# Kernel tuning notes

Hardware: AMD Instinct MI355X
Metric: run time of the kernel (lower is better)

## Reference

```python
import jax, jax.numpy as jnp
from jax import lax
import numpy as np


def _conv(x, w, b, groups=1):
    # x: NCHW, w: OIHW, stride 1, SAME padding
    y = lax.conv_general_dilated(x, w, (1, 1), 'SAME',
                                 dimension_numbers=('NCHW', 'OIHW', 'NCHW'),
                                 feature_group_count=groups)
    return y + b[None, :, None, None]


def setup_inputs() -> dict:
    key = jax.random.key(0)
    ks = jax.random.split(key, 9)
    B, C, H, W, N, K = 8, 64, 256, 256, 10, 64
    f = lambda k, s, sc=0.05: jax.random.normal(k, s, dtype=jnp.float32) * sc
    return dict(
        x=jax.random.normal(ks[0], (B, C, H, W), dtype=jnp.float32),
        ln_g=jnp.ones((C,), jnp.float32), ln_b=jnp.zeros((C,), jnp.float32),
        conv3_w=f(ks[1], (C, C, 3, 3)), conv3_b=jnp.zeros((C,), jnp.float32),
        dw_w=f(ks[2], (C, 1, 3, 3)), dw_b=jnp.zeros((C,), jnp.float32),
        c1_w=f(ks[3], (C, C, 1, 1)), c1_b=jnp.zeros((C,), jnp.float32),
        c2_w=f(ks[4], (N, C, 1, 1)), c2_b=jnp.zeros((N,), jnp.float32),
        base=f(ks[5], (N, K, K), 1.0),
        up_w=f(ks[6], (K, C, 3, 3)), up_b=jnp.zeros((K,), jnp.float32),
        down_w=f(ks[7], (C, K, 3, 3)), down_b=jnp.zeros((C,), jnp.float32),
    )


def reference(x, ln_g, ln_b, conv3_w, conv3_b, dw_w, dw_b, c1_w, c1_b,
              c2_w, c2_b, base, up_w, up_b, down_w, down_b):
    eps = 1e-5
    # LayerNorm over channel dim (permute(0,2,3,1) -> LN(last) -> permute back)
    mu = jnp.mean(x, axis=1, keepdims=True)
    var = jnp.var(x, axis=1, keepdims=True)
    xn = (x - mu) / jnp.sqrt(var + eps) * ln_g[None, :, None, None] + ln_b[None, :, None, None]
    x1 = jax.nn.gelu(_conv(xn, conv3_w, conv3_b), approximate=False)
    # predict module: dwconv -> GAP -> 1x1 -> relu -> 1x1 -> softmax over N
    C = x.shape[1]
    p = _conv(x1, dw_w, dw_b, groups=C)
    p = jnp.mean(p, axis=(2, 3), keepdims=True)           # [B,C,1,1]
    p = jax.nn.relu(_conv(p, c1_w, c1_b))
    p = _conv(p, c2_w, c2_b)[:, :, 0, 0]                  # [B,N]
    w = jax.nn.softmax(p, axis=1)                         # [B,N]
    # blend N basis KxK matrices per sample
    Wm = jnp.einsum('bn,nkl->bkl', w, base)               # [B,K,K]
    xm = _conv(x1, up_w, up_b)                            # [B,K,H,W]
    B, K, H, Wd = xm.shape
    xm = jnp.einsum('bkl,bkm->blm', Wm, xm.reshape(B, K, H * Wd)).reshape(B, K, H, Wd)
    xm = _conv(xm, down_w, down_b)                        # [B,C,H,W]
    return x + xm
```

## Files before the change

kernel.cpp:

```cpp
#include <hip/hip_runtime.h>
#include <math.h>

constexpr int B = 8, C = 64, H = 256, W = 256, HWc = H * W, N = 10;

typedef short bf8 __attribute__((ext_vector_type(8)));
typedef float f4  __attribute__((ext_vector_type(4)));
typedef unsigned short ushort;

__device__ __forceinline__ ushort f2bf(float f) {
  unsigned u = __builtin_bit_cast(unsigned, f);
  unsigned r = (u + 0x7fffu + ((u >> 16) & 1u)) >> 16;
  return (ushort)r;
}
__device__ __forceinline__ float bf2f(ushort h) {
  unsigned u = ((unsigned)h) << 16;
  return __builtin_bit_cast(float, u);
}

__global__ __launch_bounds__(256) void ln_k(
    const float* __restrict__ x, const float* __restrict__ g,
    const float* __restrict__ bt, ushort* __restrict__ xn) {
  int pix = blockIdx.x * 256 + threadIdx.x;
  int b = blockIdx.y;
  const float* xp = x + (size_t)b * C * HWc + pix;
  float v[64];
  float s = 0.f, s2 = 0.f;
#pragma unroll
  for (int c = 0; c < 64; c++) {
    v[c] = xp[(size_t)c * HWc];
    s += v[c]; s2 += v[c] * v[c];
  }
  float mu = s * (1.f / 64);
  float var = s2 * (1.f / 64) - mu * mu;
  float rstd = rsqrtf(var + 1e-5f);
  ushort* op = xn + ((size_t)b * HWc + pix) * 64;
#pragma unroll
  for (int ch = 0; ch < 8; ch++) {
    union { ushort us[8]; int4 v4; } pk;
#pragma unroll
    for (int j = 0; j < 8; j++) {
      int c = ch * 8 + j;
      pk.us[j] = f2bf((v[c] - mu) * rstd * g[c] + bt[c]);
    }
    *reinterpret_cast<int4*>(op + ch * 8) = pk.v4;
  }
}

__global__ void prep_w(const float* __restrict__ w3, const float* __restrict__ wu,
                       const float* __restrict__ wd, ushort* __restrict__ frags) {
  int idx = blockIdx.x * 256 + threadIdx.x;
  if (idx >= 3 * 4608) return;
  int conv = idx / 4608, r = idx % 4608;
  int s = r >> 8, cf = (r >> 6) & 3, lane = r & 63;
  const float* w = (conv == 0) ? w3 : (conv == 1) ? wu : wd;
  int co = (cf << 4) + (lane & 15);
  int tap = s >> 1;
  ushort* o = frags + conv * 36864 + ((size_t)r) * 8;
#pragma unroll
  for (int j = 0; j < 8; j++) {
    int ci = ((s & 1) << 5) + ((lane >> 4) << 3) + j;
    o[j] = f2bf(w[(co * 64 + ci) * 9 + tap]);
  }
}

struct Stg { int4 v[6]; };

__device__ __forceinline__ void stage_load(
    Stg& s, const ushort* __restrict__ in, int b, int h0, int w0,
    int ch2, int tid) {
#pragma unroll
  for (int it = 0; it < 6; it++) {
    int idx = it * 256 + tid;
    int4 v = make_int4(0, 0, 0, 0);
    if (idx < 1296) {
      int pix = idx >> 2, ch = idx & 3;
      int r = pix / 18, c = pix % 18;
      int gh = h0 + r - 1, gw = w0 + c - 1;
      if (gh >= 0 && gh < H && gw >= 0 && gw < W)
        v = *reinterpret_cast<const int4*>(
            in + (((size_t)b * H + gh) * W + gw) * 64 + ch2 * 32 + ch * 8);
    }
    s.v[it] = v;
  }
}

__device__ __forceinline__ void stage_write(const Stg& s, char* lds, int tid) {
#pragma unroll
  for (int it = 0; it < 6; it++) {
    int idx = it * 256 + tid;
    if (idx < 1296) {
      int pix = idx >> 2, ch = idx & 3;
      int c = pix % 18;
      int off = ((pix << 6) + (ch << 4)) ^ (((c >> 1) & 3) << 4);
      *reinterpret_cast<int4*>(lds + off) = s.v[it];
    }
  }
}

__device__ __forceinline__ void compute_half(
    const char* lds, const bf8* __restrict__ wf, int ch2,
    int wave, int lm, int lk, f4 (&acc)[16]) {
#pragma unroll
  for (int dx = 0; dx < 3; dx++) {
    bf8 wb3[3];
#pragma unroll
    for (int dy = 0; dy < 3; dy++) {
      int s = ((dy * 3 + dx) << 1) | ch2;
      wb3[dy] = wf[(s * 4 + wave) * 64 + (lk << 4) + lm];
    }
    int lc = lm + dx;
    int swz = ((lc >> 1) & 3) << 4;
#pragma unroll
    for (int hf = 0; hf < 2; hf++) {
      bf8 a[10];
#pragma unroll
      for (int r = 0; r < 10; r++) {
        int row = hf * 8 + r;
        int off = (((row * 18 + lc) << 6) + (lk << 4)) ^ swz;
        a[r] = *reinterpret_cast<const bf8*>(lds + off);
      }
#pragma unroll
      for (int dy = 0; dy < 3; dy++)
#pragma unroll
        for (int f = 0; f < 8; f++)
          acc[hf * 8 + f] =
              __builtin_amdgcn_mfma_f32_16x16x32_bf16(a[f + dy], wb3[dy], acc[hf * 8 + f], 0, 0, 0);
    }
  }
}

__device__ __forceinline__ void red_at(
    float* ldsf, const float (&a)[8], float* __restrict__ stats9,
    int k, int b, int tid) {
  __syncthreads();
#pragma unroll
  for (int j = 0; j < 8; j++) ldsf[j * 256 + tid] = a[j];
  __syncthreads();
  if (tid < 64) {
    float s = 0.f;
#pragma unroll
    for (int kk = 0; kk < 32; kk++) s += ldsf[(tid & 7) * 256 + kk * 8 + (tid >> 3)];
    atomicAdd(&stats9[(b * 64 + tid) * 9 + k], s);
  }
}

template <int ACT, int OM, int DOST>
__global__ __launch_bounds__(256, 2) void conv_mfma(
    const ushort* __restrict__ in, const ushort* __restrict__ wfrag,
    const float* __restrict__ bias, const float* __restrict__ resid,
    ushort* __restrict__ outb, float* __restrict__ outf,
    float* __restrict__ stats9) {
  __shared__ char lds[2 * 20736];
  char* ldsA = lds;
  char* ldsB = lds + 20736;
  int tid = threadIdx.x;
  int b = blockIdx.z;
  int h0 = blockIdx.y * 16, w0 = blockIdx.x * 16;
  int wave = tid >> 6, lane = tid & 63;
  int lm = lane & 15, lk = lane >> 4;
  const bf8* wf = reinterpret_cast<const bf8*>(wfrag);

  f4 acc[16];
  {
    float bv = bias[(wave << 4) + lm];
    f4 ini = {bv, bv, bv, bv};
#pragma unroll
    for (int f = 0; f < 16; f++) acc[f] = ini;
  }

  {
    Stg s0;
    stage_load(s0, in, b, h0, w0, 0, tid);
    stage_write(s0, ldsA, tid);
    __syncthreads();
  }
  {
    Stg s1;
    stage_load(s1, in, b, h0, w0, 1, tid);
    compute_half(ldsA, wf, 0, wave, lm, lk, acc);
    stage_write(s1, ldsB, tid);
    __syncthreads();
  }
  compute_half(ldsB, wf, 1, wave, lm, lk, acc);

  float* ldsf = reinterpret_cast<float*>(ldsA);
  if (OM == 0) {
    float s8[8];
    if (DOST) {
#pragma unroll
      for (int j = 0; j < 8; j++) s8[j] = 0.f;
    }
    for (int q = 0; q < 4; q++) {
      __syncthreads();
#pragma unroll
      for (int fr = 0; fr < 4; fr++) {
        int f = q * 4 + fr;
        int co = (wave << 4) + lm;
#pragma unroll
        for (int r = 0; r < 4; r++) {
          int p = (lk << 2) + r;
          ldsf[fr * 1024 + p * 64 + (co ^ ((p & 12) << 2))] = acc[f][r];
        }
      }
      __syncthreads();
#pragma unroll
      for (int i = 0; i < 2; i++) {
        int q2 = i * 256 + tid;
        int co8 = q2 & 7, p = (q2 >> 3) & 15, fr = q2 >> 7;
        int cb = (co8 * 8) ^ ((p & 12) << 2);
        f4 v0 = *reinterpret_cast<f4*>(&ldsf[fr * 1024 + p * 64 + cb]);
        f4 v1 = *reinterpret_cast<f4*>(&ldsf[fr * 1024 + p * 64 + cb + 4]);
        float vv[8] = {v0[0], v0[1], v0[2], v0[3], v1[0], v1[1], v1[2], v1[3]};
        union { ushort us[8]; int4 i4; } pk;
#pragma unroll
        for (int j = 0; j < 8; j++) {
          float v = vv[j];
          if (ACT) v = 0.5f * v * (1.f + erff(v * 0.70710678118654752f));
          if (DOST) s8[j] += v;
          pk.us[j] = f2bf(v);
        }
        *reinterpret_cast<int4*>(
            outb + (((size_t)b * H + h0 + q * 4 + fr) * W + w0 + p) * 64 + co8 * 8) = pk.i4;
      }
    }
    if (DOST) red_at(ldsf, s8, stats9, 0, b, tid);
  } else {
    for (int q = 0; q < 4; q++) {
      __syncthreads();
      if (wave == q) {
#pragma unroll
        for (int f = 0; f < 16; f++) {
          int pxl = (f << 4) + (lk << 2);
          int pxs = pxl ^ ((lm & 7) << 2);
          *reinterpret_cast<f4*>(&ldsf[lm * 256 + pxs]) = acc[f];
        }
      }
      float4 rv[4];
#pragma unroll
      for (int i = 0; i < 4; i++) {
        int q2 = i * 256 + tid;
        int chunk = q2 & 63, co16 = q2 >> 6;
        int pq = chunk * 4;
        int co = q * 16 + co16;
        size_t o = ((size_t)(b * 64 + co)) * HWc +
                   (size_t)(h0 + (pq >> 4)) * W + w0 + (pq & 15);
        rv[i] = *reinterpret_cast<const float4*>(resid + o);
      }
      __syncthreads();
#pragma unroll
      for (int i = 0; i < 4; i++) {
        int q2 = i * 256 + tid;
        int chunk = q2 & 63, co16 = q2 >> 6;
        int pq = chunk * 4;
        int pxs = pq ^ ((co16 & 7) << 2);
        f4 v = *reinterpret_cast<f4*>(&ldsf[co16 * 256 + pxs]);
        int co = q * 16 + co16;
        size_t o = ((size_t)(b * 64 + co)) * HWc +
                   (size_t)(h0 + (pq >> 4)) * W + w0 + (pq & 15);
        float4 ov;
        ov.x = v[0] + rv[i].x; ov.y = v[1] + rv[i].y;
        ov.z = v[2] + rv[i].z; ov.w = v[3] + rv[i].w;
        *reinterpret_cast<float4*>(outf + o) = ov;
      }
    }
  }
}

__global__ __launch_bounds__(256) void edge_k(const ushort* __restrict__ x1,
                                              float* __restrict__ stats9) {
  int b = blockIdx.x;
  int t = threadIdx.x;
  __shared__ float red[256];
  const size_t bb = (size_t)b * HWc * 64;
#pragma unroll
  for (int st = 0; st < 4; st++) {
    float s = 0.f;
    for (int i = 0; i < 64; i++) {
      int idx = i * 256 + t;
      int pix = idx >> 6, c = idx & 63;
      size_t off;
      if (st == 0)      off = ((size_t)pix) * 64 + c;
      else if (st == 1) off = ((size_t)(H - 1) * W + pix) * 64 + c;
      else if (st == 2) off = ((size_t)pix * W) * 64 + c;
      else              off = ((size_t)pix * W + (W - 1)) * 64 + c;
      s += bf2f(x1[bb + off]);
    }
    red[t] = s;
    __syncthreads();
    if (t < 64) {
      float v = red[t] + red[t + 64] + red[t + 128] + red[t + 192];
      stats9[(b * 64 + t) * 9 + 1 + st] = v;
    }
    __syncthreads();
  }
  if (t < 64) {
    stats9[(b * 64 + t) * 9 + 5] = bf2f(x1[bb + t]);
    stats9[(b * 64 + t) * 9 + 6] = bf2f(x1[bb + ((size_t)(W - 1)) * 64 + t]);
    stats9[(b * 64 + t) * 9 + 7] = bf2f(x1[bb + ((size_t)(H - 1) * W) * 64 + t]);
    stats9[(b * 64 + t) * 9 + 8] = bf2f(x1[bb + ((size_t)(H - 1) * W + W - 1) * 64 + t]);
  }
}

__global__ __launch_bounds__(256, 2) void upmix_mfma(
    const ushort* __restrict__ in, const ushort* __restrict__ wfrag,
    const float* __restrict__ bias, const ushort* __restrict__ wmf,
    ushort* __restrict__ out) {
  __shared__ char ldsS[20736];
  __shared__ char ldsX[32768];
  int tid = threadIdx.x;
  int b = blockIdx.z;
  int h0 = blockIdx.y * 16, w0 = blockIdx.x * 16;
  int wave = tid >> 6, lane = tid & 63;
  int lm = lane & 15, lk = lane >> 4;
  const bf8* wf = reinterpret_cast<const bf8*>(wfrag);

  const bf8* wmb = reinterpret_cast<const bf8*>(wmf + (size_t)b * 4096);
  bf8 wm[2];
#pragma unroll
  for (int s = 0; s < 2; s++) wm[s] = wmb[(s * 4 + wave) * 64 + lane];

  f4 acc[16];
  {
    float bv = bias[(wave << 4) + lm];
    f4 ini = {bv, bv, bv, bv};
#pragma unroll
    for (int f = 0; f < 16; f++) acc[f] = ini;
  }

  {
    Stg s0;
    stage_load(s0, in, b, h0, w0, 0, tid);
    stage_write(s0, ldsS, tid);
    __syncthreads();
  }
  {
    Stg s1;
    stage_load(s1, in, b, h0, w0, 1, tid);
    compute_half(ldsS, wf, 0, wave, lm, lk, acc);
    stage_write(s1, ldsX, tid);
    __syncthreads();
  }
  compute_half(ldsX, wf, 1, wave, lm, lk, acc);
  __syncthreads();

#pragma unroll
  for (int f = 0; f < 16; f++) {
#pragma unroll
    for (int r = 0; r < 4; r++) {
      int pc = (lk << 2) + r;
      int pix = (f << 4) + pc;
      int off = ((pix << 7) + ((wave << 4) + lm) * 2) ^ ((pc & 7) << 4);
      *reinterpret_cast<ushort*>(ldsX + off) = f2bf(acc[f][r]);
    }
  }
  __syncthreads();

  f4 acc2[16];
#pragma unroll
  for (int f = 0; f < 16; f++) acc2[f] = (f4){0.f, 0.f, 0.f, 0.f};
#pragma unroll
  for (int s = 0; s < 2; s++) {
    int kbyte = ((s << 5) + (lk << 3)) << 1;
#pragma unroll
    for (int f = 0; f < 16; f++) {
      int off = ((((f << 4) + lm) << 7) + kbyte) ^ ((lm & 7) << 4);
      bf8 a = *reinterpret_cast<const bf8*>(ldsX + off);
      acc2[f] = __builtin_amdgcn_mfma_f32_16x16x32_bf16(a, wm[s], acc2[f], 0, 0, 0);
    }
  }

  float* ldsf = reinterpret_cast<float*>(ldsS);
  for (int q = 0; q < 4; q++) {
    __syncthreads();
#pragma unroll
    for (int fr = 0; fr < 4; fr++) {
      int f = q * 4 + fr;
      int co = (wave << 4) + lm;
#pragma unroll
      for (int r = 0; r < 4; r++) {
        int p = (lk << 2) + r;
        ldsf[fr * 1024 + p * 64 + (co ^ ((p & 12) << 2))] = acc2[f][r];
      }
    }
    __syncthreads();
#pragma unroll
    for (int i = 0; i < 2; i++) {
      int q2 = i * 256 + tid;
      int co8 = q2 & 7, p = (q2 >> 3) & 15, fr = q2 >> 7;
      int cb = (co8 * 8) ^ ((p & 12) << 2);
      f4 v0 = *reinterpret_cast<f4*>(&ldsf[fr * 1024 + p * 64 + cb]);
      f4 v1 = *reinterpret_cast<f4*>(&ldsf[fr * 1024 + p * 64 + cb + 4]);
      float vv[8] = {v0[0], v0[1], v0[2], v0[3], v1[0], v1[1], v1[2], v1[3]};
      union { ushort us[8]; int4 i4; } pk;
#pragma unroll
      for (int j = 0; j < 8; j++) pk.us[j] = f2bf(vv[j]);
      *reinterpret_cast<int4*>(
          out + (((size_t)b * H + h0 + q * 4 + fr) * W + w0 + p) * 64 + co8 * 8) = pk.i4;
    }
  }
}

__global__ void mlp_k(const float* __restrict__ stats9, const float* __restrict__ dww,
                      const float* __restrict__ dwb,
                      const float* __restrict__ c1w, const float* __restrict__ c1b,
                      const float* __restrict__ c2w, const float* __restrict__ c2b,
                      const float* __restrict__ basep, ushort* __restrict__ wmf) {
  int b = blockIdx.x;
  int t = threadIdx.x;
  __shared__ float pm[64], p1[64], p2[16];
  {
    const float* st = stats9 + (b * 64 + t) * 9;
    float S = st[0], R0 = st[1], Rh = st[2], C0 = st[3], Cw = st[4];
    float X00 = st[5], X0w = st[6], Xh0 = st[7], Xhw = st[8];
    float acc = 0.f;
#pragma unroll
    for (int ky = 0; ky < 3; ky++)
#pragma unroll
      for (int kx = 0; kx < 3; kx++) {
        float T = S;
        if (ky == 2) T -= R0;
        if (ky == 0) T -= Rh;
        if (kx == 2) T -= C0;
        if (kx == 0) T -= Cw;
        if (ky == 2 && kx == 2) T += X00;
        if (ky == 2 && kx == 0) T += X0w;
        if (ky == 0 && kx == 2) T += Xh0;
        if (ky == 0 && kx == 0) T += Xhw;
        acc += dww[t * 9 + ky * 3 + kx] * T;
      }
    pm[t] = acc * (1.f / HWc) + dwb[t];
  }
  __syncthreads();
  float a = c1b[t];
  for (int ci = 0; ci < 64; ci++) a += pm[ci] * c1w[t * 64 + ci];
  p1[t] = fmaxf(a, 0.f);
  __syncthreads();
  if (t < N) {
    float a2 = c2b[t];
    for (int ci = 0; ci < 64; ci++) a2 += p1[ci] * c2w[t * 64 + ci];
    p2[t] = a2;
  }
  __syncthreads();
  float m = -1e30f;
  for (int n = 0; n < N; n++) m = fmaxf(m, p2[n]);
  float e[N], s = 0.f;
  for (int n = 0; n < N; n++) { e[n] = expf(p2[n] - m); s += e[n]; }
  float inv = 1.f / s;
  for (int idx = t; idx < 4096; idx += 64) {
    int j = idx & 7, lane = (idx >> 3) & 63, cf = (idx >> 9) & 3, s2 = idx >> 11;
    int k = (s2 << 5) + ((lane >> 4) << 3) + j;
    int l = (cf << 4) + (lane & 15);
    float acc = 0.f;
    for (int n = 0; n < N; n++) acc += e[n] * inv * basep[n * 4096 + k * 64 + l];
    wmf[(size_t)b * 4096 + idx] = f2bf(acc);
  }
}

__global__ void zero_k(float* p, int n) {
  int i = blockIdx.x * 256 + threadIdx.x;
  if (i < n) p[i] = 0.f;
}

extern "C" void kernel_launch(void* const* d_in, const int* in_sizes, int n_in,
                              void* d_out, int out_size, void* d_ws, size_t ws_size,
                              hipStream_t stream) {
  const float* x       = (const float*)d_in[0];
  const float* ln_g    = (const float*)d_in[1];
  const float* ln_b    = (const float*)d_in[2];
  const float* conv3_w = (const float*)d_in[3];
  const float* conv3_b = (const float*)d_in[4];
  const float* dw_w    = (const float*)d_in[5];
  const float* dw_b    = (const float*)d_in[6];
  const float* c1_w    = (const float*)d_in[7];
  const float* c1_b    = (const float*)d_in[8];
  const float* c2_w    = (const float*)d_in[9];
  const float* c2_b    = (const float*)d_in[10];
  const float* basep   = (const float*)d_in[11];
  const float* up_w    = (const float*)d_in[12];
  const float* up_b    = (const float*)d_in[13];
  const float* down_w  = (const float*)d_in[14];
  const float* down_b  = (const float*)d_in[15];
  float* out = (float*)d_out;

  char* wsb = (char*)d_ws;
  size_t big = (size_t)B * HWc * 64 * sizeof(ushort);
  ushort* bufA   = (ushort*)wsb;
  ushort* bufB   = (ushort*)(wsb + big);
  ushort* wfrags = (ushort*)(wsb + 2 * big);
  ushort* wmfrag = (ushort*)(wsb + 2 * big + 3 * 36864 * 2);
  float*  stats  = (float*)(wsb + 2 * big + 3 * 36864 * 2 + 8 * 4096 * 2);

  prep_w<<<54, 256, 0, stream>>>(conv3_w, up_w, down_w, wfrags);
  zero_k<<<18, 256, 0, stream>>>(stats, B * 64 * 9);
  ln_k<<<dim3(HWc / 256, B), 256, 0, stream>>>(x, ln_g, ln_b, bufA);
  conv_mfma<1, 0, 1><<<dim3(16, 16, B), 256, 0, stream>>>(
      bufA, wfrags + 0 * 36864, conv3_b, nullptr, bufB, nullptr, stats);
  edge_k<<<B, 256, 0, stream>>>(bufB, stats);
  mlp_k<<<B, 64, 0, stream>>>(stats, dw_w, dw_b, c1_w, c1_b, c2_w, c2_b, basep, wmfrag);
  upmix_mfma<<<dim3(16, 16, B), 256, 0, stream>>>(
      bufB, wfrags + 1 * 36864, up_b, wmfrag, bufA);
  conv_mfma<0, 1, 0><<<dim3(16, 16, B), 256, 0, stream>>>(
      bufA, wfrags + 2 * 36864, down_b, x, nullptr, out, stats);
}
```

Before: 331.5 us.

## Fuse edge stats into MLP kernel, write residual output directly, halve epilogue passes

Folds the edge/corner statistics kernel into the MLP kernel, which now runs 256 threads and keeps the intermediates in shared memory, so one launch and the global stats round-trip go away. The final conv epilogue no longer transposes through LDS: each lane reads the residual and writes float4 output straight from its accumulators. The bf16 epilogues of conv3 and upmix stage 8 rows per pass instead of 4, which halves the barrier rounds but uses more LDS. The direct residual path gives less coalesced 16-byte accesses per row in exchange for dropping the LDS shuffle and its syncs.

```diff
diff --git a/kernel.cpp b/kernel.cpp
--- a/kernel.cpp
+++ b/kernel.cpp
@@ -130,8 +130,8 @@
 }
 
 __device__ __forceinline__ void red_at(
-    float* ldsf, const float (&a)[8], float* __restrict__ stats9,
-    int k, int b, int tid) {
+    float* ldsf, const float (&a)[8], float* __restrict__ Ssum,
+    int b, int tid) {
   __syncthreads();
 #pragma unroll
   for (int j = 0; j < 8; j++) ldsf[j * 256 + tid] = a[j];
@@ -140,7 +140,7 @@
     float s = 0.f;
 #pragma unroll
     for (int kk = 0; kk < 32; kk++) s += ldsf[(tid & 7) * 256 + kk * 8 + (tid >> 3)];
-    atomicAdd(&stats9[(b * 64 + tid) * 9 + k], s);
+    atomicAdd(&Ssum[b * 64 + tid], s);
   }
 }
 
@@ -149,7 +149,7 @@
     const ushort* __restrict__ in, const ushort* __restrict__ wfrag,
     const float* __restrict__ bias, const float* __restrict__ resid,
     ushort* __restrict__ outb, float* __restrict__ outf,
-    float* __restrict__ stats9) {
+    float* __restrict__ Ssum) {
   __shared__ char lds[2 * 20736];
   char* ldsA = lds;
   char* ldsB = lds + 20736;
@@ -183,18 +183,18 @@
   }
   compute_half(ldsB, wf, 1, wave, lm, lk, acc);
 
-  float* ldsf = reinterpret_cast<float*>(ldsA);
   if (OM == 0) {
+    float* ldsf = reinterpret_cast<float*>(lds);
     float s8[8];
     if (DOST) {
 #pragma unroll
       for (int j = 0; j < 8; j++) s8[j] = 0.f;
     }
-    for (int q = 0; q < 4; q++) {
+    for (int h2 = 0; h2 < 2; h2++) {
       __syncthreads();
 #pragma unroll
-      for (int fr = 0; fr < 4; fr++) {
-        int f = q * 4 + fr;
+      for (int fr = 0; fr < 8; fr++) {
+        int f = h2 * 8 + fr;
         int co = (wave << 4) + lm;
 #pragma unroll
         for (int r = 0; r < 4; r++) {
@@ -204,7 +204,7 @@
       }
       __syncthreads();
 #pragma unroll
-      for (int i = 0; i < 2; i++) {
+      for (int i = 0; i < 4; i++) {
         int q2 = i * 256 + tid;
         int co8 = q2 & 7, p = (q2 >> 3) & 15, fr = q2 >> 7;
         int cb = (co8 * 8) ^ ((p & 12) << 2);
@@ -220,84 +220,26 @@
           pk.us[j] = f2bf(v);
         }
         *reinterpret_cast<int4*>(
-            outb + (((size_t)b * H + h0 + q * 4 + fr) * W + w0 + p) * 64 + co8 * 8) = pk.i4;
+            outb + (((size_t)b * H + h0 + h2 * 8 + fr) * W + w0 + p) * 64 + co8 * 8) = pk.i4;
       }
     }
-    if (DOST) red_at(ldsf, s8, stats9, 0, b, tid);
+    if (DOST) red_at(ldsf, s8, Ssum, b, tid);
   } else {
-    for (int q = 0; q < 4; q++) {
-      __syncthreads();
-      if (wave == q) {
-#pragma unroll
-        for (int f = 0; f < 16; f++) {
-          int pxl = (f << 4) + (lk << 2);
-          int pxs = pxl ^ ((lm & 7) << 2);
-          *reinterpret_cast<f4*>(&ldsf[lm * 256 + pxs]) = acc[f];
-        }
-      }
-      float4 rv[4];
-#pragma unroll
-      for (int i = 0; i < 4; i++) {
-        int q2 = i * 256 + tid;
-        int chunk = q2 & 63, co16 = q2 >> 6;
-        int pq = chunk * 4;
-        int co = q * 16 + co16;
-        size_t o = ((size_t)(b * 64 + co)) * HWc +
-                   (size_t)(h0 + (pq >> 4)) * W + w0 + (pq & 15);
-        rv[i] = *reinterpret_cast<const float4*>(resid + o);
-      }
-      __syncthreads();
-#pragma unroll
-      for (int i = 0; i < 4; i++) {
-        int q2 = i * 256 + tid;
-        int chunk = q2 & 63, co16 = q2 >> 6;
-        int pq = chunk * 4;
-        int pxs = pq ^ ((co16 & 7) << 2);
-        f4 v = *reinterpret_cast<f4*>(&ldsf[co16 * 256 + pxs]);
-        int co = q * 16 + co16;
-        size_t o = ((size_t)(b * 64 + co)) * HWc +
-                   (size_t)(h0 + (pq >> 4)) * W + w0 + (pq & 15);
-        float4 ov;
-        ov.x = v[0] + rv[i].x; ov.y = v[1] + rv[i].y;
-        ov.z = v[2] + rv[i].z; ov.w = v[3] + rv[i].w;
-        *reinterpret_cast<float4*>(outf + o) = ov;
-      }
-    }
-  }
-}
-
-__global__ __launch_bounds__(256) void edge_k(const ushort* __restrict__ x1,
-                                              float* __restrict__ stats9) {
-  int b = blockIdx.x;
-  int t = threadIdx.x;
-  __shared__ float red[256];
-  const size_t bb = (size_t)b * HWc * 64;
-#pragma unroll
-  for (int st = 0; st < 4; st++) {
-    float s = 0.f;
-    for (int i = 0; i < 64; i++) {
-      int idx = i * 256 + t;
-      int pix = idx >> 6, c = idx & 63;
-      size_t off;
-      if (st == 0)      off = ((size_t)pix) * 64 + c;
-      else if (st == 1) off = ((size_t)(H - 1) * W + pix) * 64 + c;
-      else if (st == 2) off = ((size_t)pix * W) * 64 + c;
-      else              off = ((size_t)pix * W + (W - 1)) * 64 + c;
-      s += bf2f(x1[bb + off]);
-    }
-    red[t] = s;
-    __syncthreads();
-    if (t < 64) {
-      float v = red[t] + red[t + 64] + red[t + 128] + red[t + 192];
-      stats9[(b * 64 + t) * 9 + 1 + st] = v;
-    }
-    __syncthreads();
-  }
-  if (t < 64) {
-    stats9[(b * 64 + t) * 9 + 5] = bf2f(x1[bb + t]);
-    stats9[(b * 64 + t) * 9 + 6] = bf2f(x1[bb + ((size_t)(W - 1)) * 64 + t]);
-    stats9[(b * 64 + t) * 9 + 7] = bf2f(x1[bb + ((size_t)(H - 1) * W) * 64 + t]);
-    stats9[(b * 64 + t) * 9 + 8] = bf2f(x1[bb + ((size_t)(H - 1) * W + W - 1) * 64 + t]);
+    int co = (wave << 4) + lm;
+    size_t base = ((size_t)(b * 64 + co)) * HWc + (size_t)h0 * W + w0 + (lk << 2);
+    float4 rv[16];
+#pragma unroll
+    for (int f = 0; f < 16; f++)
+      rv[f] = *reinterpret_cast<const float4*>(resid + base + (size_t)f * W);
+#pragma unroll
+    for (int f = 0; f < 16; f++) {
+      float4 ov;
+      ov.x = acc[f][0] + rv[f].x;
+      ov.y = acc[f][1] + rv[f].y;
+      ov.z = acc[f][2] + rv[f].z;
+      ov.w = acc[f][3] + rv[f].w;
+      *reinterpret_cast<float4*>(outf + base + (size_t)f * W) = ov;
+    }
   }
 }
 
@@ -369,12 +311,12 @@
     }
   }
 
-  float* ldsf = reinterpret_cast<float*>(ldsS);
-  for (int q = 0; q < 4; q++) {
-    __syncthreads();
-#pragma unroll
-    for (int fr = 0; fr < 4; fr++) {
-      int f = q * 4 + fr;
+  float* ldsf = reinterpret_cast<float*>(ldsX);
+  for (int h2 = 0; h2 < 2; h2++) {
+    __syncthreads();
+#pragma unroll
+    for (int fr = 0; fr < 8; fr++) {
+      int f = h2 * 8 + fr;
       int co = (wave << 4) + lm;
 #pragma unroll
       for (int r = 0; r < 4; r++) {
@@ -384,7 +326,7 @@
     }
     __syncthreads();
 #pragma unroll
-    for (int i = 0; i < 2; i++) {
+    for (int i = 0; i < 4; i++) {
       int q2 = i * 256 + tid;
       int co8 = q2 & 7, p = (q2 >> 3) & 15, fr = q2 >> 7;
       int cb = (co8 * 8) ^ ((p & 12) << 2);
@@ -395,23 +337,52 @@
 #pragma unroll
       for (int j = 0; j < 8; j++) pk.us[j] = f2bf(vv[j]);
       *reinterpret_cast<int4*>(
-          out + (((size_t)b * H + h0 + q * 4 + fr) * W + w0 + p) * 64 + co8 * 8) = pk.i4;
-    }
-  }
-}
-
-__global__ void mlp_k(const float* __restrict__ stats9, const float* __restrict__ dww,
-                      const float* __restrict__ dwb,
-                      const float* __restrict__ c1w, const float* __restrict__ c1b,
-                      const float* __restrict__ c2w, const float* __restrict__ c2b,
-                      const float* __restrict__ basep, ushort* __restrict__ wmf) {
+          out + (((size_t)b * H + h0 + h2 * 8 + fr) * W + w0 + p) * 64 + co8 * 8) = pk.i4;
+    }
+  }
+}
+
+__global__ __launch_bounds__(256) void mlp_k(
+    const ushort* __restrict__ x1, const float* __restrict__ Ssum,
+    const float* __restrict__ dww, const float* __restrict__ dwb,
+    const float* __restrict__ c1w, const float* __restrict__ c1b,
+    const float* __restrict__ c2w, const float* __restrict__ c2b,
+    const float* __restrict__ basep, ushort* __restrict__ wmf) {
   int b = blockIdx.x;
   int t = threadIdx.x;
+  __shared__ float red[256];
+  __shared__ float eg[4][64], corn[4][64];
   __shared__ float pm[64], p1[64], p2[16];
-  {
-    const float* st = stats9 + (b * 64 + t) * 9;
-    float S = st[0], R0 = st[1], Rh = st[2], C0 = st[3], Cw = st[4];
-    float X00 = st[5], X0w = st[6], Xh0 = st[7], Xhw = st[8];
+  const size_t bb = (size_t)b * HWc * 64;
+#pragma unroll
+  for (int st = 0; st < 4; st++) {
+    float s = 0.f;
+    for (int i = 0; i < 64; i++) {
+      int idx = i * 256 + t;
+      int pix = idx >> 6, c = idx & 63;
+      size_t off;
+      if (st == 0)      off = ((size_t)pix) * 64 + c;
+      else if (st == 1) off = ((size_t)(H - 1) * W + pix) * 64 + c;
+      else if (st == 2) off = ((size_t)pix * W) * 64 + c;
+      else              off = ((size_t)pix * W + (W - 1)) * 64 + c;
+      s += bf2f(x1[bb + off]);
+    }
+    red[t] = s;
+    __syncthreads();
+    if (t < 64) eg[st][t] = red[t] + red[t + 64] + red[t + 128] + red[t + 192];
+    __syncthreads();
+  }
+  if (t < 64) {
+    corn[0][t] = bf2f(x1[bb + t]);
+    corn[1][t] = bf2f(x1[bb + ((size_t)(W - 1)) * 64 + t]);
+    corn[2][t] = bf2f(x1[bb + ((size_t)(H - 1) * W) * 64 + t]);
+    corn[3][t] = bf2f(x1[bb + ((size_t)(H - 1) * W + W - 1) * 64 + t]);
+  }
+  __syncthreads();
+  if (t < 64) {
+    float S = Ssum[b * 64 + t];
+    float R0 = eg[0][t], Rh = eg[1][t], C0 = eg[2][t], Cw = eg[3][t];
+    float X00 = corn[0][t], X0w = corn[1][t], Xh0 = corn[2][t], Xhw = corn[3][t];
     float acc = 0.f;
 #pragma unroll
     for (int ky = 0; ky < 3; ky++)
@@ -431,9 +402,11 @@
     pm[t] = acc * (1.f / HWc) + dwb[t];
   }
   __syncthreads();
-  float a = c1b[t];
-  for (int ci = 0; ci < 64; ci++) a += pm[ci] * c1w[t * 64 + ci];
-  p1[t] = fmaxf(a, 0.f);
+  if (t < 64) {
+    float a = c1b[t];
+    for (int ci = 0; ci < 64; ci++) a += pm[ci] * c1w[t * 64 + ci];
+    p1[t] = fmaxf(a, 0.f);
+  }
   __syncthreads();
   if (t < N) {
     float a2 = c2b[t];
@@ -443,15 +416,15 @@
   __syncthreads();
   float m = -1e30f;
   for (int n = 0; n < N; n++) m = fmaxf(m, p2[n]);
-  float e[N], s = 0.f;
-  for (int n = 0; n < N; n++) { e[n] = expf(p2[n] - m); s += e[n]; }
+  float ev[N], s = 0.f;
+  for (int n = 0; n < N; n++) { ev[n] = expf(p2[n] - m); s += ev[n]; }
   float inv = 1.f / s;
-  for (int idx = t; idx < 4096; idx += 64) {
+  for (int idx = t; idx < 4096; idx += 256) {
     int j = idx & 7, lane = (idx >> 3) & 63, cf = (idx >> 9) & 3, s2 = idx >> 11;
     int k = (s2 << 5) + ((lane >> 4) << 3) + j;
     int l = (cf << 4) + (lane & 15);
     float acc = 0.f;
-    for (int n = 0; n < N; n++) acc += e[n] * inv * basep[n * 4096 + k * 64 + l];
+    for (int n = 0; n < N; n++) acc += ev[n] * inv * basep[n * 4096 + k * 64 + l];
     wmf[(size_t)b * 4096 + idx] = f2bf(acc);
   }
 }
@@ -488,17 +461,17 @@
   ushort* bufB   = (ushort*)(wsb + big);
   ushort* wfrags = (ushort*)(wsb + 2 * big);
   ushort* wmfrag = (ushort*)(wsb + 2 * big + 3 * 36864 * 2);
-  float*  stats  = (float*)(wsb + 2 * big + 3 * 36864 * 2 + 8 * 4096 * 2);
+  float*  Ssum   = (float*)(wsb + 2 * big + 3 * 36864 * 2 + 8 * 4096 * 2);
 
   prep_w<<<54, 256, 0, stream>>>(conv3_w, up_w, down_w, wfrags);
-  zero_k<<<18, 256, 0, stream>>>(stats, B * 64 * 9);
+  zero_k<<<2, 256, 0, stream>>>(Ssum, B * 64);
   ln_k<<<dim3(HWc / 256, B), 256, 0, stream>>>(x, ln_g, ln_b, bufA);
   conv_mfma<1, 0, 1><<<dim3(16, 16, B), 256, 0, stream>>>(
-      bufA, wfrags + 0 * 36864, conv3_b, nullptr, bufB, nullptr, stats);
-  edge_k<<<B, 256, 0, stream>>>(bufB, stats);
-  mlp_k<<<B, 64, 0, stream>>>(stats, dw_w, dw_b, c1_w, c1_b, c2_w, c2_b, basep, wmfrag);
+      bufA, wfrags + 0 * 36864, conv3_b, nullptr, bufB, nullptr, Ssum);
+  mlp_k<<<B, 256, 0, stream>>>(bufB, Ssum, dw_w, dw_b, c1_w, c1_b, c2_w, c2_b,
+                               basep, wmfrag);
   upmix_mfma<<<dim3(16, 16, B), 256, 0, stream>>>(
       bufB, wfrags + 1 * 36864, up_b, wmfrag, bufA);
   conv_mfma<0, 1, 0><<<dim3(16, 16, B), 256, 0, stream>>>(
-      bufA, wfrags + 2 * 36864, down_b, x, nullptr, out, stats);
-}
+      bufA, wfrags + 2 * 36864, down_b, x, nullptr, out, Ssum);
+}
```

Result: no change. 326.4 us (-1.5%).
